# Performance work log

Measured on AMD Instinct MI355X. Metric: run time of the kernel, lower is better.

Reference implementation:

```python
import jax, jax.numpy as jnp
import numpy as np
import math

B, S, D, H = 4, 1024, 1024, 16
DK = D // H


def setup_inputs() -> dict:
    key = jax.random.key(0)
    ks = jax.random.split(key, 12)
    scale = 1.0 / math.sqrt(D)
    inp = {
        "query": jax.random.normal(ks[0], (B, S, D), jnp.float32),
        "key": jax.random.normal(ks[1], (B, S, D), jnp.float32),
        "value": jax.random.normal(ks[2], (B, S, D), jnp.float32),
        "mask": jnp.ones((B, S, S), jnp.int32),
        "Wq": jax.random.uniform(ks[3], (D, D), jnp.float32, -scale, scale),
        "bq": jax.random.uniform(ks[4], (D,), jnp.float32, -scale, scale),
        "Wk": jax.random.uniform(ks[5], (D, D), jnp.float32, -scale, scale),
        "bk": jax.random.uniform(ks[6], (D,), jnp.float32, -scale, scale),
        "Wv": jax.random.uniform(ks[7], (D, D), jnp.float32, -scale, scale),
        "bv": jax.random.uniform(ks[8], (D,), jnp.float32, -scale, scale),
        "Wo": jax.random.uniform(ks[9], (D, D), jnp.float32, -scale, scale),
        "bo": jax.random.uniform(ks[10], (D,), jnp.float32, -scale, scale),
    }
    return inp


def reference(query, key, value, mask, Wq, bq, Wk, bk, Wv, bv, Wo, bo):
    b, s, d = query.shape
    # QKV projections (torch Linear: x @ W.T + b), split into heads -> [b, h, s, dk]
    def proj(x, W, bias):
        return (x @ W.T + bias).reshape(b, -1, H, DK).transpose(0, 2, 1, 3)

    q = proj(query, Wq, bq)
    k = proj(key, Wk, bk)
    v = proj(value, Wv, bv)

    scores = jnp.einsum("bhqd,bhkd->bhqk", q, k) / jnp.sqrt(jnp.float32(DK))
    scores = jnp.where(mask[:, None, :, :] == 0, jnp.float32(-1e9), scores)
    p_attn = jax.nn.softmax(scores, axis=-1)  # dropout p=0.0 -> identity

    x = jnp.einsum("bhqk,bhkd->bhqd", p_attn, v)
    x = x.transpose(0, 2, 1, 3).reshape(b, -1, H * DK)  # [b, s, d]
    # F.threshold(x, 0.2, 0.0): values <= 0.2 replaced with 0
    x = jnp.where(x > 0.2, x, jnp.float32(0.0))
    x1 = x @ Wo.T + bo
    x1 = jnp.mean(x1, axis=-1, keepdims=True)
    return x + x1
```

## Files before the change

kernel.cpp:

```cpp
#include <hip/hip_runtime.h>
#include <hip/hip_bf16.h>
#include <math.h>

#define BB 4
#define SS 1024
#define DD 1024
#define NH 16
#define DKH 64

typedef __attribute__((ext_vector_type(8))) short bf16x8;
typedef __attribute__((ext_vector_type(4))) float f32x4;

__device__ __forceinline__ ushort f2bf(float f) {
  __hip_bfloat16 h = __float2bfloat16(f);
  return *(ushort*)&h;
}

__device__ __forceinline__ bf16x8 pack8(float4 a, float4 b) {
  bf16x8 r;
  r[0] = (short)f2bf(a.x); r[1] = (short)f2bf(a.y);
  r[2] = (short)f2bf(a.z); r[3] = (short)f2bf(a.w);
  r[4] = (short)f2bf(b.x); r[5] = (short)f2bf(b.y);
  r[6] = (short)f2bf(b.z); r[7] = (short)f2bf(b.w);
  return r;
}

__device__ __forceinline__ void async16(const void* g, void* l) {
  __builtin_amdgcn_global_load_lds(
      (const __attribute__((address_space(1))) unsigned int*)g,
      (__attribute__((address_space(3))) unsigned int*)l, 16, 0, 0);
}

__global__ __launch_bounds__(256) void prep_all(
    const float* __restrict__ Xq, const float* __restrict__ Xk, const float* __restrict__ Xv,
    const int* __restrict__ mask,
    const float* __restrict__ Wq, const float* __restrict__ Wk, const float* __restrict__ Wv,
    const float* __restrict__ Wo, const float* __restrict__ bo,
    ushort* __restrict__ Wb, ushort* __restrict__ Ab,
    float* __restrict__ wo_sum, float* __restrict__ bo_mean,
    int* __restrict__ maskOK) {
  __shared__ int smi[4];
  const int bid = blockIdx.x;
  const int tid = threadIdx.x;

  if (bid < 64) {
    const int row0 = bid * 16;
    float4 acc = make_float4(0.f, 0.f, 0.f, 0.f);
#pragma unroll
    for (int r = 0; r < 16; ++r) {
      const float4 v = *(const float4*)(Wo + (size_t)(row0 + r) * DD + tid * 4);
      acc.x += v.x; acc.y += v.y; acc.z += v.z; acc.w += v.w;
    }
    atomicAdd(&wo_sum[tid * 4 + 0], acc.x);
    atomicAdd(&wo_sum[tid * 4 + 1], acc.y);
    atomicAdd(&wo_sum[tid * 4 + 2], acc.z);
    atomicAdd(&wo_sum[tid * 4 + 3], acc.w);
    return;
  }

  if (bid == 64) {
    if (tid < 64) {
      float s = 0.f;
      for (int i = tid; i < 1024; i += 64) s += bo[i];
#pragma unroll
      for (int off = 1; off < 64; off <<= 1) s += __shfl_xor(s, off);
      if (tid == 0) *bo_mean = s * (1.0f / 1024.0f);
    }
    return;
  }

  if (bid < 577) {
    const int m = bid - 65;
    const int kt = m & 15, qt = (m >> 4) & 7, b = m >> 7;
    const int row = tid >> 1, half = tid & 1;
    const int* p = mask + ((size_t)b * SS + qt * 128 + row) * SS + kt * 64 + half * 32;
    int ok = 1;
#pragma unroll
    for (int j = 0; j < 8; ++j) {
      const int4 mm = *(const int4*)(p + j * 4);
      ok &= (mm.x != 0) & (mm.y != 0) & (mm.z != 0) & (mm.w != 0);
    }
    const unsigned long long bal = __ballot(ok);
    if ((tid & 63) == 0) smi[tid >> 6] = (bal == ~0ULL) ? 1 : 0;
    __syncthreads();
    if (tid == 0) maskOK[(b * 8 + qt) * 16 + kt] = smi[0] & smi[1] & smi[2] & smi[3];
    return;
  }

  if (bid < 6721) {
    const size_t g = (size_t)(bid - 577) * 2048 + (size_t)tid * 8;
    const int t = (int)(g >> 22);
    const float* base = (t == 0) ? Xq : (t == 1) ? Xk : Xv;
    const size_t off = g & 4194303;
    const float4 f0 = *(const float4*)(base + off);
    const float4 f1 = *(const float4*)(base + off + 4);
    *(bf16x8*)(Ab + g) = pack8(f0, f1);
    return;
  }

  {
    const size_t g = (size_t)(bid - 6721) * 2048 + (size_t)tid * 8;
    const int t = (int)(g >> 20);
    const float* W = (t == 0) ? Wq : (t == 1) ? Wk : Wv;
    const size_t off = g & 1048575;
    const float4 f0 = *(const float4*)(W + off);
    const float4 f1 = *(const float4*)(W + off + 4);
    *(bf16x8*)(Wb + g) = pack8(f0, f1);
  }
}

__global__ __launch_bounds__(256) void gemm_qkv_bf16(
    const ushort* __restrict__ Ab, const ushort* __restrict__ Wb,
    const float* __restrict__ bq, const float* __restrict__ bk, const float* __restrict__ bv,
    ushort* __restrict__ QKVb) {
  const int z = blockIdx.z;
  const char* A = (const char*)(Ab + (size_t)z * 4194304);
  const char* W = (const char*)(Wb + (size_t)z * 1048576);
  const float* bias = (z == 0) ? bq : (z == 1) ? bk : bv;
  ushort* Cz = QKVb + (size_t)z * 4194304;
  const float sc = (z == 0) ? 0.125f : 1.0f;

  __shared__ ushort As[8192];
  __shared__ ushort Ws[8192];

  const int tid = threadIdx.x;
  const int lane = tid & 63, w = tid >> 6;
  const int quad = lane >> 4, l15 = lane & 15;
  const int wn = w & 1, wm = w >> 1;
  const int m0 = blockIdx.x * 128, n0 = blockIdx.y * 128;

  const int r8 = lane >> 3;
  const int cg = (lane & 7) ^ r8;
  const int xr = l15 & 7;

  f32x4 acc[4][4];
  const f32x4 z4 = {0.f, 0.f, 0.f, 0.f};
#pragma unroll
  for (int mt = 0; mt < 4; ++mt)
#pragma unroll
    for (int nt = 0; nt < 4; ++nt) acc[mt][nt] = z4;

  for (int k0 = 0; k0 < DD; k0 += 64) {
    __syncthreads();
#pragma unroll
    for (int t = 0; t < 4; ++t) {
      const int grp = w * 4 + t;
      const int row = grp * 8 + r8;
      async16(A + ((size_t)(m0 + row) * DD + k0 + cg * 8) * 2, &As[grp * 512]);
      async16(W + ((size_t)(n0 + row) * DD + k0 + cg * 8) * 2, &Ws[grp * 512]);
    }
    __syncthreads();
#pragma unroll
    for (int kk = 0; kk < 2; ++kk) {
      const int qp = (kk * 4 + quad) ^ xr;
      bf16x8 wf[4], af[4];
#pragma unroll
      for (int nt = 0; nt < 4; ++nt)
        wf[nt] = *(const bf16x8*)&Ws[(wn * 64 + nt * 16 + l15) * 64 + qp * 8];
#pragma unroll
      for (int mt = 0; mt < 4; ++mt)
        af[mt] = *(const bf16x8*)&As[(wm * 64 + mt * 16 + l15) * 64 + qp * 8];
#pragma unroll
      for (int mt = 0; mt < 4; ++mt)
#pragma unroll
        for (int nt = 0; nt < 4; ++nt)
          acc[mt][nt] = __builtin_amdgcn_mfma_f32_16x16x32_bf16(wf[nt], af[mt], acc[mt][nt], 0, 0, 0);
    }
  }

#pragma unroll
  for (int nt = 0; nt < 4; ++nt) {
    const float4 b4 = *(const float4*)(bias + n0 + wn * 64 + nt * 16 + quad * 4);
#pragma unroll
    for (int mt = 0; mt < 4; ++mt) {
      const f32x4 v = acc[mt][nt];
      ushort4 pk;
      pk.x = f2bf((v[0] + b4.x) * sc);
      pk.y = f2bf((v[1] + b4.y) * sc);
      pk.z = f2bf((v[2] + b4.z) * sc);
      pk.w = f2bf((v[3] + b4.w) * sc);
      *(ushort4*)&Cz[(size_t)(m0 + wm * 64 + mt * 16 + l15) * DD + n0 + wn * 64 + nt * 16 + quad * 4] = pk;
    }
  }
}

__global__ __launch_bounds__(256) void flash_mfma(
    const ushort* __restrict__ QKVb, const int* __restrict__ mask,
    const int* __restrict__ maskOK, float* __restrict__ X) {
  __shared__ ushort Vt[64 * 72];
  __shared__ ushort Ps[128 * 72];

  const ushort* Qb = QKVb;
  const ushort* Kb = QKVb + 4194304;
  const ushort* Vb = QKVb + 8388608;

  const int tid = threadIdx.x;
  const int lane = tid & 63, w = tid >> 6;
  const int quad = lane >> 4, l15 = lane & 15;
  const int h = blockIdx.x, qblk = blockIdx.y, b = blockIdx.z;
  const int qbase = qblk * 128 + w * 32;

  bf16x8 qf[2][2];
#pragma unroll
  for (int qt = 0; qt < 2; ++qt)
#pragma unroll
    for (int ks = 0; ks < 2; ++ks)
      qf[qt][ks] = *(const bf16x8*)(Qb + (size_t)(b * SS + qbase + qt * 16 + l15) * DD +
                                    h * DKH + ks * 32 + quad * 8);

  f32x4 o[4][2];
  const f32x4 z4 = {0.f, 0.f, 0.f, 0.f};
#pragma unroll
  for (int dt = 0; dt < 4; ++dt)
#pragma unroll
    for (int qt = 0; qt < 2; ++qt) o[dt][qt] = z4;
  float l_run[2] = {0.f, 0.f};

  const int vp = tid & 31;
  const int vdc = tid >> 5;
  const ushort* Vg = Vb + (size_t)(b * SS) * DD + h * DKH + vdc * 8;
  const ushort* Kg = Kb + (size_t)(b * SS) * DD + h * DKH;
  uint* VtU = (uint*)Vt;
  const int* Mb = mask + (size_t)b * SS * SS;

  for (int kt = 0; kt < 16; ++kt) {
    const int k064 = kt * 64;
    __syncthreads();

    bf16x8 kf[4][2];
#pragma unroll
    for (int mt = 0; mt < 4; ++mt)
#pragma unroll
      for (int ks = 0; ks < 2; ++ks)
        kf[mt][ks] = *(const bf16x8*)(Kg + (size_t)(k064 + mt * 16 + l15) * DD +
                                      ks * 32 + quad * 8);

    union { uint4 u; ushort s[8]; } v0, v1;
    v0.u = *(const uint4*)(Vg + (size_t)(k064 + 2 * vp) * DD);
    v1.u = *(const uint4*)(Vg + (size_t)(k064 + 2 * vp + 1) * DD);
#pragma unroll
    for (int j = 0; j < 8; ++j)
      VtU[(vdc * 8 + j) * 36 + vp] = (uint)v0.s[j] | ((uint)v1.s[j] << 16);
    __syncthreads();

    f32x4 s[4][2];
#pragma unroll
    for (int mt = 0; mt < 4; ++mt)
#pragma unroll
      for (int qt = 0; qt < 2; ++qt) {
        f32x4 a = z4;
        a = __builtin_amdgcn_mfma_f32_16x16x32_bf16(kf[mt][0], qf[qt][0], a, 0, 0, 0);
        a = __builtin_amdgcn_mfma_f32_16x16x32_bf16(kf[mt][1], qf[qt][1], a, 0, 0, 0);
        s[mt][qt] = a;
      }

    const int ok = maskOK[(b * 8 + qblk) * 16 + kt];
    if (!ok) {
#pragma unroll
      for (int mt = 0; mt < 4; ++mt)
#pragma unroll
        for (int qt = 0; qt < 2; ++qt)
#pragma unroll
          for (int reg = 0; reg < 4; ++reg) {
            const int q = qbase + qt * 16 + l15;
            const int key = k064 + mt * 16 + quad * 4 + reg;
            if (Mb[(size_t)q * SS + key] == 0) s[mt][qt][reg] = -1e9f;
          }
    }

#pragma unroll
    for (int qt = 0; qt < 2; ++qt) {
      float rs = 0.f;
#pragma unroll
      for (int mt = 0; mt < 4; ++mt) {
#pragma unroll
        for (int reg = 0; reg < 4; ++reg) {
          const float p = __expf(s[mt][qt][reg]);
          s[mt][qt][reg] = p;
          rs += p;
        }
      }
      l_run[qt] += rs;
#pragma unroll
      for (int mt = 0; mt < 4; ++mt) {
        ushort4 pk;
        pk.x = f2bf(s[mt][qt][0]);
        pk.y = f2bf(s[mt][qt][1]);
        pk.z = f2bf(s[mt][qt][2]);
        pk.w = f2bf(s[mt][qt][3]);
        *(ushort4*)&Ps[(w * 32 + qt * 16 + l15) * 72 + mt * 16 + quad * 4] = pk;
      }
    }

    bf16x8 pf[2][2];
#pragma unroll
    for (int qt = 0; qt < 2; ++qt)
#pragma unroll
      for (int ks = 0; ks < 2; ++ks)
        pf[qt][ks] = *(const bf16x8*)&Ps[(w * 32 + qt * 16 + l15) * 72 + ks * 32 + quad * 8];
#pragma unroll
    for (int dt = 0; dt < 4; ++dt) {
      bf16x8 vf0 = *(const bf16x8*)&Vt[(dt * 16 + l15) * 72 + quad * 8];
      bf16x8 vf1 = *(const bf16x8*)&Vt[(dt * 16 + l15) * 72 + 32 + quad * 8];
#pragma unroll
      for (int qt = 0; qt < 2; ++qt) {
        o[dt][qt] = __builtin_amdgcn_mfma_f32_16x16x32_bf16(vf0, pf[qt][0], o[dt][qt], 0, 0, 0);
        o[dt][qt] = __builtin_amdgcn_mfma_f32_16x16x32_bf16(vf1, pf[qt][1], o[dt][qt], 0, 0, 0);
      }
    }
  }

#pragma unroll
  for (int qt = 0; qt < 2; ++qt) {
    float l = l_run[qt];
    l += __shfl_xor(l, 16);
    l += __shfl_xor(l, 32);
    const float inv = 1.0f / l;
#pragma unroll
    for (int dt = 0; dt < 4; ++dt) {
      const f32x4 ov = o[dt][qt] * inv;
      *(f32x4*)(X + (size_t)(b * SS + qbase + qt * 16 + l15) * DD +
                h * DKH + dt * 16 + quad * 4) = ov;
    }
  }
}

__global__ __launch_bounds__(256) void epilogue_kernel(float* __restrict__ X,
                                                       const float* __restrict__ wo_sum,
                                                       const float* __restrict__ bo_mean) {
  __shared__ float red[4];
  const int row = blockIdx.x;
  const int tid = threadIdx.x;
  float* xr = X + (size_t)row * DD;
  const float4 x = *(const float4*)(xr + tid * 4);
  const float4 w = *(const float4*)(wo_sum + tid * 4);
  float4 xt;
  xt.x = (x.x > 0.2f) ? x.x : 0.f;
  xt.y = (x.y > 0.2f) ? x.y : 0.f;
  xt.z = (x.z > 0.2f) ? x.z : 0.f;
  xt.w = (x.w > 0.2f) ? x.w : 0.f;
  float part = xt.x * w.x + xt.y * w.y + xt.z * w.z + xt.w * w.w;
#pragma unroll
  for (int off = 1; off < 64; off <<= 1) part += __shfl_xor(part, off);
  if ((tid & 63) == 0) red[tid >> 6] = part;
  __syncthreads();
  const float x1 = ((red[0] + red[1]) + (red[2] + red[3])) * (1.0f / 1024.0f) + *bo_mean;
  const float4 o = make_float4(xt.x + x1, xt.y + x1, xt.z + x1, xt.w + x1);
  *(float4*)(xr + tid * 4) = o;
}

extern "C" void kernel_launch(void* const* d_in, const int* in_sizes, int n_in,
                              void* d_out, int out_size, void* d_ws, size_t ws_size,
                              hipStream_t stream) {
  const float* Xq = (const float*)d_in[0];
  const float* Xk = (const float*)d_in[1];
  const float* Xv = (const float*)d_in[2];
  const int* mask = (const int*)d_in[3];
  const float* Wq = (const float*)d_in[4];
  const float* bq = (const float*)d_in[5];
  const float* Wk = (const float*)d_in[6];
  const float* bk = (const float*)d_in[7];
  const float* Wv = (const float*)d_in[8];
  const float* bv = (const float*)d_in[9];
  const float* Wo = (const float*)d_in[10];
  const float* bo = (const float*)d_in[11];

  ushort* Wb = (ushort*)d_ws;
  ushort* Ab = Wb + (size_t)3 * 1048576;
  ushort* QKVb = Ab + (size_t)3 * 4194304;
  float* wo_sum = (float*)(QKVb + (size_t)3 * 4194304);
  float* bo_mean = wo_sum + 1024;
  int* maskOK = (int*)(bo_mean + 1);
  float* X = (float*)d_out;

  hipMemsetAsync(wo_sum, 0, 1024 * sizeof(float), stream);

  prep_all<<<8257, 256, 0, stream>>>(Xq, Xk, Xv, mask, Wq, Wk, Wv, Wo, bo,
                                     Wb, Ab, wo_sum, bo_mean, maskOK);

  gemm_qkv_bf16<<<dim3(32, 8, 3), 256, 0, stream>>>(Ab, Wb, bq, bk, bv, QKVb);

  flash_mfma<<<dim3(16, 8, 4), 256, 0, stream>>>(QKVb, mask, maskOK, X);

  epilogue_kernel<<<4096, 256, 0, stream>>>(X, wo_sum, bo_mean);
}
```

Before: 225.4 us.

## Double-buffer QKV GEMM, halve flash query tile, batch prep and epilogue rows

The QKV GEMM now double-buffers its LDS tiles with a K-step of 32. The next tile is issued asynchronously while the current one is computed, which hides global load latency and removes one barrier per iteration. The flash attention kernel handles 64 queries per block instead of 128, doubling the grid to 1024 blocks for better CU occupancy at the cost of re-reading K/V more often. The prep kernel does 8 conversion chunks per thread, and the epilogue handles 4 rows per block, cutting block count and launch overhead.

```diff
diff --git a/kernel.cpp b/kernel.cpp
--- a/kernel.cpp
+++ b/kernel.cpp
@@ -87,25 +87,33 @@
     return;
   }
 
-  if (bid < 6721) {
-    const size_t g = (size_t)(bid - 577) * 2048 + (size_t)tid * 8;
-    const int t = (int)(g >> 22);
-    const float* base = (t == 0) ? Xq : (t == 1) ? Xk : Xv;
-    const size_t off = g & 4194303;
-    const float4 f0 = *(const float4*)(base + off);
-    const float4 f1 = *(const float4*)(base + off + 4);
-    *(bf16x8*)(Ab + g) = pack8(f0, f1);
+  if (bid < 1345) {
+    const int c0 = bid - 577;
+#pragma unroll
+    for (int it = 0; it < 8; ++it) {
+      const size_t g = (size_t)(c0 + it * 768) * 2048 + (size_t)tid * 8;
+      const int t = (int)(g >> 22);
+      const float* base = (t == 0) ? Xq : (t == 1) ? Xk : Xv;
+      const size_t off = g & 4194303;
+      const float4 f0 = *(const float4*)(base + off);
+      const float4 f1 = *(const float4*)(base + off + 4);
+      *(bf16x8*)(Ab + g) = pack8(f0, f1);
+    }
     return;
   }
 
   {
-    const size_t g = (size_t)(bid - 6721) * 2048 + (size_t)tid * 8;
-    const int t = (int)(g >> 20);
-    const float* W = (t == 0) ? Wq : (t == 1) ? Wk : Wv;
-    const size_t off = g & 1048575;
-    const float4 f0 = *(const float4*)(W + off);
-    const float4 f1 = *(const float4*)(W + off + 4);
-    *(bf16x8*)(Wb + g) = pack8(f0, f1);
+    const int c0 = bid - 1345;
+#pragma unroll
+    for (int it = 0; it < 8; ++it) {
+      const size_t g = (size_t)(c0 + it * 192) * 2048 + (size_t)tid * 8;
+      const int t = (int)(g >> 20);
+      const float* W = (t == 0) ? Wq : (t == 1) ? Wk : Wv;
+      const size_t off = g & 1048575;
+      const float4 f0 = *(const float4*)(W + off);
+      const float4 f1 = *(const float4*)(W + off + 4);
+      *(bf16x8*)(Wb + g) = pack8(f0, f1);
+    }
   }
 }
 
@@ -120,8 +128,8 @@
   ushort* Cz = QKVb + (size_t)z * 4194304;
   const float sc = (z == 0) ? 0.125f : 1.0f;
 
-  __shared__ ushort As[8192];
-  __shared__ ushort Ws[8192];
+  __shared__ ushort As[2][4096];
+  __shared__ ushort Ws[2][4096];
 
   const int tid = threadIdx.x;
   const int lane = tid & 63, w = tid >> 6;
@@ -129,9 +137,9 @@
   const int wn = w & 1, wm = w >> 1;
   const int m0 = blockIdx.x * 128, n0 = blockIdx.y * 128;
 
-  const int r8 = lane >> 3;
-  const int cg = (lane & 7) ^ r8;
-  const int xr = l15 & 7;
+  const int r4 = lane >> 2;
+  const int gc = (lane & 3) ^ (r4 & 3);
+  const int rc = quad ^ (l15 & 3);
 
   f32x4 acc[4][4];
   const f32x4 z4 = {0.f, 0.f, 0.f, 0.f};
@@ -140,32 +148,33 @@
 #pragma unroll
     for (int nt = 0; nt < 4; ++nt) acc[mt][nt] = z4;
 
-  for (int k0 = 0; k0 < DD; k0 += 64) {
+  auto stage = [&](int k0, int buf) {
+#pragma unroll
+    for (int j = 0; j < 2; ++j) {
+      const int grp = w * 2 + j;
+      const int row = grp * 16 + r4;
+      async16(A + ((size_t)(m0 + row) * DD + k0 + gc * 8) * 2, &As[buf][grp * 512]);
+      async16(W + ((size_t)(n0 + row) * DD + k0 + gc * 8) * 2, &Ws[buf][grp * 512]);
+    }
+  };
+
+  stage(0, 0);
+  for (int k0 = 0; k0 < DD; k0 += 32) {
+    const int buf = (k0 >> 5) & 1;
     __syncthreads();
-#pragma unroll
-    for (int t = 0; t < 4; ++t) {
-      const int grp = w * 4 + t;
-      const int row = grp * 8 + r8;
-      async16(A + ((size_t)(m0 + row) * DD + k0 + cg * 8) * 2, &As[grp * 512]);
-      async16(W + ((size_t)(n0 + row) * DD + k0 + cg * 8) * 2, &Ws[grp * 512]);
-    }
-    __syncthreads();
-#pragma unroll
-    for (int kk = 0; kk < 2; ++kk) {
-      const int qp = (kk * 4 + quad) ^ xr;
-      bf16x8 wf[4], af[4];
+    if (k0 + 32 < DD) stage(k0 + 32, buf ^ 1);
+    bf16x8 wf[4], af[4];
+#pragma unroll
+    for (int nt = 0; nt < 4; ++nt)
+      wf[nt] = *(const bf16x8*)&Ws[buf][(wn * 64 + nt * 16 + l15) * 32 + rc * 8];
+#pragma unroll
+    for (int mt = 0; mt < 4; ++mt)
+      af[mt] = *(const bf16x8*)&As[buf][(wm * 64 + mt * 16 + l15) * 32 + rc * 8];
+#pragma unroll
+    for (int mt = 0; mt < 4; ++mt)
 #pragma unroll
       for (int nt = 0; nt < 4; ++nt)
-        wf[nt] = *(const bf16x8*)&Ws[(wn * 64 + nt * 16 + l15) * 64 + qp * 8];
-#pragma unroll
-      for (int mt = 0; mt < 4; ++mt)
-        af[mt] = *(const bf16x8*)&As[(wm * 64 + mt * 16 + l15) * 64 + qp * 8];
-#pragma unroll
-      for (int mt = 0; mt < 4; ++mt)
-#pragma unroll
-        for (int nt = 0; nt < 4; ++nt)
-          acc[mt][nt] = __builtin_amdgcn_mfma_f32_16x16x32_bf16(wf[nt], af[mt], acc[mt][nt], 0, 0, 0);
-    }
+        acc[mt][nt] = __builtin_amdgcn_mfma_f32_16x16x32_bf16(wf[nt], af[mt], acc[mt][nt], 0, 0, 0);
   }
 
 #pragma unroll
@@ -188,7 +197,7 @@
     const ushort* __restrict__ QKVb, const int* __restrict__ mask,
     const int* __restrict__ maskOK, float* __restrict__ X) {
   __shared__ ushort Vt[64 * 72];
-  __shared__ ushort Ps[128 * 72];
+  __shared__ ushort Ps[64 * 72];
 
   const ushort* Qb = QKVb;
   const ushort* Kb = QKVb + 4194304;
@@ -198,23 +207,19 @@
   const int lane = tid & 63, w = tid >> 6;
   const int quad = lane >> 4, l15 = lane & 15;
   const int h = blockIdx.x, qblk = blockIdx.y, b = blockIdx.z;
-  const int qbase = qblk * 128 + w * 32;
-
-  bf16x8 qf[2][2];
-#pragma unroll
-  for (int qt = 0; qt < 2; ++qt)
-#pragma unroll
-    for (int ks = 0; ks < 2; ++ks)
-      qf[qt][ks] = *(const bf16x8*)(Qb + (size_t)(b * SS + qbase + qt * 16 + l15) * DD +
-                                    h * DKH + ks * 32 + quad * 8);
-
-  f32x4 o[4][2];
+  const int qbase = qblk * 64 + w * 16;
+
+  bf16x8 qf[2];
+#pragma unroll
+  for (int ks = 0; ks < 2; ++ks)
+    qf[ks] = *(const bf16x8*)(Qb + (size_t)(b * SS + qbase + l15) * DD +
+                              h * DKH + ks * 32 + quad * 8);
+
+  f32x4 o[4];
   const f32x4 z4 = {0.f, 0.f, 0.f, 0.f};
 #pragma unroll
-  for (int dt = 0; dt < 4; ++dt)
-#pragma unroll
-    for (int qt = 0; qt < 2; ++qt) o[dt][qt] = z4;
-  float l_run[2] = {0.f, 0.f};
+  for (int dt = 0; dt < 4; ++dt) o[dt] = z4;
+  float l_run = 0.f;
 
   const int vp = tid & 31;
   const int vdc = tid >> 5;
@@ -243,83 +248,70 @@
       VtU[(vdc * 8 + j) * 36 + vp] = (uint)v0.s[j] | ((uint)v1.s[j] << 16);
     __syncthreads();
 
-    f32x4 s[4][2];
-#pragma unroll
-    for (int mt = 0; mt < 4; ++mt)
-#pragma unroll
-      for (int qt = 0; qt < 2; ++qt) {
-        f32x4 a = z4;
-        a = __builtin_amdgcn_mfma_f32_16x16x32_bf16(kf[mt][0], qf[qt][0], a, 0, 0, 0);
-        a = __builtin_amdgcn_mfma_f32_16x16x32_bf16(kf[mt][1], qf[qt][1], a, 0, 0, 0);
-        s[mt][qt] = a;
+    f32x4 s[4];
+#pragma unroll
+    for (int mt = 0; mt < 4; ++mt) {
+      f32x4 a = z4;
+      a = __builtin_amdgcn_mfma_f32_16x16x32_bf16(kf[mt][0], qf[0], a, 0, 0, 0);
+      a = __builtin_amdgcn_mfma_f32_16x16x32_bf16(kf[mt][1], qf[1], a, 0, 0, 0);
+      s[mt] = a;
+    }
+
+    const int ok = maskOK[(b * 8 + (qblk >> 1)) * 16 + kt];
+    if (!ok) {
+#pragma unroll
+      for (int mt = 0; mt < 4; ++mt)
+#pragma unroll
+        for (int reg = 0; reg < 4; ++reg) {
+          const int q = qbase + l15;
+          const int key = k064 + mt * 16 + quad * 4 + reg;
+          if (Mb[(size_t)q * SS + key] == 0) s[mt][reg] = -1e9f;
+        }
+    }
+
+    float rs = 0.f;
+#pragma unroll
+    for (int mt = 0; mt < 4; ++mt) {
+#pragma unroll
+      for (int reg = 0; reg < 4; ++reg) {
+        const float p = __expf(s[mt][reg]);
+        s[mt][reg] = p;
+        rs += p;
       }
-
-    const int ok = maskOK[(b * 8 + qblk) * 16 + kt];
-    if (!ok) {
-#pragma unroll
-      for (int mt = 0; mt < 4; ++mt)
-#pragma unroll
-        for (int qt = 0; qt < 2; ++qt)
-#pragma unroll
-          for (int reg = 0; reg < 4; ++reg) {
-            const int q = qbase + qt * 16 + l15;
-            const int key = k064 + mt * 16 + quad * 4 + reg;
-            if (Mb[(size_t)q * SS + key] == 0) s[mt][qt][reg] = -1e9f;
-          }
-    }
-
-#pragma unroll
-    for (int qt = 0; qt < 2; ++qt) {
-      float rs = 0.f;
-#pragma unroll
-      for (int mt = 0; mt < 4; ++mt) {
-#pragma unroll
-        for (int reg = 0; reg < 4; ++reg) {
-          const float p = __expf(s[mt][qt][reg]);
-          s[mt][qt][reg] = p;
-          rs += p;
-        }
-      }
-      l_run[qt] += rs;
-#pragma unroll
-      for (int mt = 0; mt < 4; ++mt) {
-        ushort4 pk;
-        pk.x = f2bf(s[mt][qt][0]);
-        pk.y = f2bf(s[mt][qt][1]);
-        pk.z = f2bf(s[mt][qt][2]);
-        pk.w = f2bf(s[mt][qt][3]);
-        *(ushort4*)&Ps[(w * 32 + qt * 16 + l15) * 72 + mt * 16 + quad * 4] = pk;
-      }
-    }
-
-    bf16x8 pf[2][2];
-#pragma unroll
-    for (int qt = 0; qt < 2; ++qt)
-#pragma unroll
-      for (int ks = 0; ks < 2; ++ks)
-        pf[qt][ks] = *(const bf16x8*)&Ps[(w * 32 + qt * 16 + l15) * 72 + ks * 32 + quad * 8];
+    }
+    l_run += rs;
+#pragma unroll
+    for (int mt = 0; mt < 4; ++mt) {
+      ushort4 pk;
+      pk.x = f2bf(s[mt][0]);
+      pk.y = f2bf(s[mt][1]);
+      pk.z = f2bf(s[mt][2]);
+      pk.w = f2bf(s[mt][3]);
+      *(ushort4*)&Ps[(w * 16 + l15) * 72 + mt * 16 + quad * 4] = pk;
+    }
+
+    bf16x8 pf[2];
+#pragma unroll
+    for (int ks = 0; ks < 2; ++ks)
+      pf[ks] = *(const bf16x8*)&Ps[(w * 16 + l15) * 72 + ks * 32 + quad * 8];
 #pragma unroll
     for (int dt = 0; dt < 4; ++dt) {
       bf16x8 vf0 = *(const bf16x8*)&Vt[(dt * 16 + l15) * 72 + quad * 8];
       bf16x8 vf1 = *(const bf16x8*)&Vt[(dt * 16 + l15) * 72 + 32 + quad * 8];
-#pragma unroll
-      for (int qt = 0; qt < 2; ++qt) {
-        o[dt][qt] = __builtin_amdgcn_mfma_f32_16x16x32_bf16(vf0, pf[qt][0], o[dt][qt], 0, 0, 0);
-        o[dt][qt] = __builtin_amdgcn_mfma_f32_16x16x32_bf16(vf1, pf[qt][1], o[dt][qt], 0, 0, 0);
-      }
-    }
-  }
-
-#pragma unroll
-  for (int qt = 0; qt < 2; ++qt) {
-    float l = l_run[qt];
+      o[dt] = __builtin_amdgcn_mfma_f32_16x16x32_bf16(vf0, pf[0], o[dt], 0, 0, 0);
+      o[dt] = __builtin_amdgcn_mfma_f32_16x16x32_bf16(vf1, pf[1], o[dt], 0, 0, 0);
+    }
+  }
+
+  {
+    float l = l_run;
     l += __shfl_xor(l, 16);
     l += __shfl_xor(l, 32);
     const float inv = 1.0f / l;
 #pragma unroll
     for (int dt = 0; dt < 4; ++dt) {
-      const f32x4 ov = o[dt][qt] * inv;
-      *(f32x4*)(X + (size_t)(b * SS + qbase + qt * 16 + l15) * DD +
+      const f32x4 ov = o[dt] * inv;
+      *(f32x4*)(X + (size_t)(b * SS + qbase + l15) * DD +
                 h * DKH + dt * 16 + quad * 4) = ov;
     }
   }
@@ -328,25 +320,32 @@
 __global__ __launch_bounds__(256) void epilogue_kernel(float* __restrict__ X,
                                                        const float* __restrict__ wo_sum,
                                                        const float* __restrict__ bo_mean) {
-  __shared__ float red[4];
-  const int row = blockIdx.x;
+  __shared__ float red[4][4];
   const int tid = threadIdx.x;
-  float* xr = X + (size_t)row * DD;
-  const float4 x = *(const float4*)(xr + tid * 4);
-  const float4 w = *(const float4*)(wo_sum + tid * 4);
-  float4 xt;
-  xt.x = (x.x > 0.2f) ? x.x : 0.f;
-  xt.y = (x.y > 0.2f) ? x.y : 0.f;
-  xt.z = (x.z > 0.2f) ? x.z : 0.f;
-  xt.w = (x.w > 0.2f) ? x.w : 0.f;
-  float part = xt.x * w.x + xt.y * w.y + xt.z * w.z + xt.w * w.w;
-#pragma unroll
-  for (int off = 1; off < 64; off <<= 1) part += __shfl_xor(part, off);
-  if ((tid & 63) == 0) red[tid >> 6] = part;
+  const float4 wv = *(const float4*)(wo_sum + tid * 4);
+  const float bm = *bo_mean;
+  float4 xt[4];
+#pragma unroll
+  for (int r = 0; r < 4; ++r) {
+    const int row = blockIdx.x * 4 + r;
+    const float4 x = *(const float4*)(X + (size_t)row * DD + tid * 4);
+    xt[r].x = (x.x > 0.2f) ? x.x : 0.f;
+    xt[r].y = (x.y > 0.2f) ? x.y : 0.f;
+    xt[r].z = (x.z > 0.2f) ? x.z : 0.f;
+    xt[r].w = (x.w > 0.2f) ? x.w : 0.f;
+    float part = xt[r].x * wv.x + xt[r].y * wv.y + xt[r].z * wv.z + xt[r].w * wv.w;
+#pragma unroll
+    for (int off = 1; off < 64; off <<= 1) part += __shfl_xor(part, off);
+    if ((tid & 63) == 0) red[r][tid >> 6] = part;
+  }
   __syncthreads();
-  const float x1 = ((red[0] + red[1]) + (red[2] + red[3])) * (1.0f / 1024.0f) + *bo_mean;
-  const float4 o = make_float4(xt.x + x1, xt.y + x1, xt.z + x1, xt.w + x1);
-  *(float4*)(xr + tid * 4) = o;
+#pragma unroll
+  for (int r = 0; r < 4; ++r) {
+    const int row = blockIdx.x * 4 + r;
+    const float x1 = ((red[r][0] + red[r][1]) + (red[r][2] + red[r][3])) * (1.0f / 1024.0f) + bm;
+    const float4 o = make_float4(xt[r].x + x1, xt[r].y + x1, xt[r].z + x1, xt[r].w + x1);
+    *(float4*)(X + (size_t)row * DD + tid * 4) = o;
+  }
 }
 
 extern "C" void kernel_launch(void* const* d_in, const int* in_sizes, int n_in,
@@ -375,12 +374,12 @@
 
   hipMemsetAsync(wo_sum, 0, 1024 * sizeof(float), stream);
 
-  prep_all<<<8257, 256, 0, stream>>>(Xq, Xk, Xv, mask, Wq, Wk, Wv, Wo, bo,
+  prep_all<<<1537, 256, 0, stream>>>(Xq, Xk, Xv, mask, Wq, Wk, Wv, Wo, bo,
                                      Wb, Ab, wo_sum, bo_mean, maskOK);
 
   gemm_qkv_bf16<<<dim3(32, 8, 3), 256, 0, stream>>>(Ab, Wb, bq, bk, bv, QKVb);
 
-  flash_mfma<<<dim3(16, 8, 4), 256, 0, stream>>>(QKVb, mask, maskOK, X);
-
-  epilogue_kernel<<<4096, 256, 0, stream>>>(X, wo_sum, bo_mean);
-}
+  flash_mfma<<<dim3(16, 16, 4), 256, 0, stream>>>(QKVb, mask, maskOK, X);
+
+  epilogue_kernel<<<1024, 256, 0, stream>>>(X, wo_sum, bo_mean);
+}
```

Result: slower. 270.8 us (+20.2%).
